# Kernel optimization log

Measured on AMD Instinct MI355X. Metric: run time of the kernel, lower is better.

Reference implementation:

```python
import jax, jax.numpy as jnp
import numpy as np
import math

BS, N, D_MODEL, H = 8, 1024, 512, 8
D_K = D_MODEL // H


def setup_inputs() -> dict:
    key = jax.random.key(0)
    ks = jax.random.split(key, 12)
    s = 1.0 / math.sqrt(D_MODEL)
    inp = {
        "query": jax.random.normal(ks[0], (BS, N, D_MODEL), jnp.float32),
        "key": jax.random.normal(ks[1], (BS, N, D_MODEL), jnp.float32),
        "value": jax.random.normal(ks[2], (BS, N, D_MODEL), jnp.float32),
        "wc_matrix": jax.random.normal(ks[3], (BS, N, N), jnp.float32),
        "Wq": jax.random.normal(ks[4], (D_MODEL, D_MODEL), jnp.float32) * s,
        "bq": jnp.zeros((D_MODEL,), jnp.float32),
        "Wk": jax.random.normal(ks[5], (D_MODEL, D_MODEL), jnp.float32) * s,
        "bk": jnp.zeros((D_MODEL,), jnp.float32),
        "Wv": jax.random.normal(ks[6], (D_MODEL, D_MODEL), jnp.float32) * s,
        "bv": jnp.zeros((D_MODEL,), jnp.float32),
        "Wo": jax.random.normal(ks[7], (D_MODEL, D_MODEL), jnp.float32) * s,
        "bo": jnp.zeros((D_MODEL,), jnp.float32),
    }
    return inp


def _split_heads(x):
    # (bs, N, d_model) -> (bs, h, N, d_k)
    b, n, _ = x.shape
    return x.reshape(b, n, H, D_K).transpose(0, 2, 1, 3)


def reference(query, key, value, wc_matrix, Wq, bq, Wk, bk, Wv, bv, Wo, bo):
    # Linear projections (torch Linear: x @ W.T + b), split into heads
    q = _split_heads(query @ Wq.T + bq)
    k = _split_heads(key @ Wk.T + bk)
    v = _split_heads(value @ Wv.T + bv)

    # scores: (bs, h, N, N)
    scores = jnp.einsum("bhnd,bhmd->bhnm", q, k) / jnp.sqrt(jnp.float32(D_K))
    # WC modulation: scores * softmax(wc)[:, None] + scores  (softmax_wc=True, residual=True)
    wc_sm = jax.nn.softmax(wc_matrix, axis=-1)[:, None]  # (bs, 1, N, N)
    scores = scores * wc_sm + scores
    p_attn = jax.nn.softmax(scores, axis=-1)  # dropout is identity in eval

    a = jnp.einsum("bhnm,bhmd->bhnd", p_attn, v)
    a = a.transpose(0, 2, 1, 3).reshape(query.shape[0], -1, D_MODEL)
    return a @ Wo.T + bo
```

## Files before the change

### kernel.cpp

```cpp
#include <hip/hip_runtime.h>
#include <math.h>


#define BS 8
#define SEQ 1024
#define DM 512
#define NH 8
#define DK 64
#define ROWS (BS * SEQ)

typedef __bf16 bf16_t;
typedef bf16_t bf16x8 __attribute__((ext_vector_type(8)));
typedef bf16_t bf16x4 __attribute__((ext_vector_type(4)));
typedef float f32x4 __attribute__((ext_vector_type(4)));

__device__ inline f32x4 mfma32(bf16x8 a, bf16x8 b, f32x4 c) {
  return __builtin_amdgcn_mfma_f32_16x16x32_bf16(a, b, c, 0, 0, 0);
}

__device__ inline void gload_lds16(const bf16_t* g, bf16_t* l) {
  __builtin_amdgcn_global_load_lds(
      (const __attribute__((address_space(1))) void*)g,
      (__attribute__((address_space(3))) void*)l, 16, 0, 0);
}

__global__ __launch_bounds__(256) void prep_kernel(
    const float* q, const float* k, const float* v,
    const float* wq, const float* wk, const float* wv, const float* wo,
    bf16_t* xq, bf16_t* xk, bf16_t* xv,
    bf16_t* wqb, bf16_t* wkb, bf16_t* wvb, bf16_t* wob,
    const float* __restrict__ wc, bf16_t* __restrict__ G) {
  int bx = blockIdx.x;
  int t = threadIdx.x;
  if (bx < 1664) {
    const float* srcs[7] = {q, k, v, wq, wk, wv, wo};
    bf16_t* dsts[7] = {xq, xk, xv, wqb, wkb, wvb, wob};
    int seg, boff;
    if (bx < 1536) { seg = bx >> 9; boff = bx & 511; }
    else { seg = 3 + ((bx - 1536) >> 5); boff = (bx - 1536) & 31; }
    const float* src = srcs[seg] + (size_t)boff * 8192;
    bf16_t* dst = dsts[seg] + (size_t)boff * 8192;
#pragma unroll
    for (int f = 0; f < 8; ++f) {
      int idx = (f * 256 + t) * 4;
      float4 x = *(const float4*)(src + idx);
      bf16x4 o;
      o[0] = (bf16_t)x.x; o[1] = (bf16_t)x.y; o[2] = (bf16_t)x.z; o[3] = (bf16_t)x.w;
      *(bf16x4*)(dst + idx) = o;
    }
  } else {
    int row = bx - 1664;
    const float* x = wc + (size_t)row * SEQ;
    bf16_t* y = G + (size_t)row * SEQ;
    float4 vv = *(const float4*)(x + t * 4);
    float m = fmaxf(fmaxf(vv.x, vv.y), fmaxf(vv.z, vv.w));
#pragma unroll
    for (int off = 32; off > 0; off >>= 1) m = fmaxf(m, __shfl_xor(m, off, 64));
    __shared__ float sm[4], ss[4];
    int w = t >> 6;
    if ((t & 63) == 0) sm[w] = m;
    __syncthreads();
    m = fmaxf(fmaxf(sm[0], sm[1]), fmaxf(sm[2], sm[3]));
    float4 e;
    e.x = __expf(vv.x - m); e.y = __expf(vv.y - m);
    e.z = __expf(vv.z - m); e.w = __expf(vv.w - m);
    float s = e.x + e.y + e.z + e.w;
#pragma unroll
    for (int off = 32; off > 0; off >>= 1) s += __shfl_xor(s, off, 64);
    if ((t & 63) == 0) ss[w] = s;
    __syncthreads();
    s = ss[0] + ss[1] + ss[2] + ss[3];
    float inv = 1.0f / s;
    const float SC = 0.18033688011112042f;
    bf16x4 g;
    g[0] = (bf16_t)((1.0f + e.x * inv) * SC);
    g[1] = (bf16_t)((1.0f + e.y * inv) * SC);
    g[2] = (bf16_t)((1.0f + e.z * inv) * SC);
    g[3] = (bf16_t)((1.0f + e.w * inv) * SC);
    *(bf16x4*)(y + t * 4) = g;
  }
}

template <int BM, bool WO>
__device__ inline void gemm_core(const bf16_t* X, const bf16_t* W,
                                 const float* bias, void* Cv,
                                 int mblk, int nblk, bool vtrans) {
  constexpr int STAGE_B = (2 * BM * 32 + 2 * 128 * 32) * 2;
  constexpr int EPI_B = WO ? BM * 132 * 4 : 128 * 136 * 2;
  constexpr int SMEM_B = STAGE_B > EPI_B ? STAGE_B : EPI_B;
  __shared__ __align__(16) char smem[SMEM_B];
  bf16_t* As = (bf16_t*)smem;
  bf16_t* Bs = (bf16_t*)smem + 2 * BM * 32;

  int t = threadIdx.x, lane = t & 63, w = t >> 6;
  int quad = lane >> 4, l15 = lane & 15;
  constexpr int MT = BM / 32;
  int m0w = (w & 1) * (BM / 2), n0w = (w >> 1) * 64;
  int mbase = mblk * BM, nbase = nblk * 128;
  int lr = lane >> 2, l4 = lane & 3;
  f32x4 acc[MT][4] = {};

#pragma unroll
  for (int f = 0; f < BM / 64; ++f) {
    int i = f * 4 + w;
    gload_lds16(X + (size_t)(mbase + i * 16 + lr) * DM + l4 * 8, &As[i * 512]);
  }
#pragma unroll
  for (int f = 0; f < 2; ++f) {
    int i = f * 4 + w;
    gload_lds16(W + (size_t)(nbase + i * 16 + lr) * DM + l4 * 8, &Bs[i * 512]);
  }

  for (int it = 0; it < 16; ++it) {
    __syncthreads();
    int cb = it & 1;
    if (it + 1 < 16) {
      int kb = (it + 1) * 32, nb = (it + 1) & 1;
#pragma unroll
      for (int f = 0; f < BM / 64; ++f) {
        int i = f * 4 + w;
        gload_lds16(X + (size_t)(mbase + i * 16 + lr) * DM + kb + l4 * 8,
                    &As[nb * BM * 32 + i * 512]);
      }
#pragma unroll
      for (int f = 0; f < 2; ++f) {
        int i = f * 4 + w;
        gload_lds16(W + (size_t)(nbase + i * 16 + lr) * DM + kb + l4 * 8,
                    &Bs[nb * 128 * 32 + i * 512]);
      }
    }
    bf16x8 af[MT], bfr[4];
#pragma unroll
    for (int mt = 0; mt < MT; ++mt)
      af[mt] = *(const bf16x8*)&As[cb * BM * 32 + (m0w + mt * 16 + l15) * 32 + quad * 8];
#pragma unroll
    for (int nt = 0; nt < 4; ++nt)
      bfr[nt] = *(const bf16x8*)&Bs[cb * 128 * 32 + (n0w + nt * 16 + l15) * 32 + quad * 8];
#pragma unroll
    for (int mt = 0; mt < MT; ++mt)
#pragma unroll
      for (int nt = 0; nt < 4; ++nt)
        acc[mt][nt] = mfma32(af[mt], bfr[nt], acc[mt][nt]);
  }

  if (WO) {
    __syncthreads();
    float* Cs = (float*)smem;
#pragma unroll
    for (int nt = 0; nt < 4; ++nt) {
      int colL = n0w + nt * 16 + l15;
      float bc = bias[nbase + colL];
#pragma unroll
      for (int mt = 0; mt < MT; ++mt)
#pragma unroll
        for (int r = 0; r < 4; ++r)
          Cs[(m0w + mt * 16 + quad * 4 + r) * 132 + colL] = acc[mt][nt][r] + bc;
    }
    __syncthreads();
    constexpr int NP = BM * 128 / 4 / 256;
#pragma unroll
    for (int p = 0; p < NP; ++p) {
      int flat = p * 256 + t;
      int row = flat >> 5, c4 = (flat & 31) * 4;
      float4 vv = *(const float4*)&Cs[row * 132 + c4];
      *(float4*)&((float*)Cv)[(size_t)(mbase + row) * DM + nbase + c4] = vv;
    }
  } else if (vtrans) {
    __syncthreads();
    bf16_t* Ts = (bf16_t*)smem;
#pragma unroll
    for (int nt = 0; nt < 4; ++nt) {
      int colL = n0w + nt * 16 + l15;
      float bc = bias[nbase + colL];
#pragma unroll
      for (int mt = 0; mt < MT; ++mt) {
        bf16x4 ov;
#pragma unroll
        for (int r = 0; r < 4; ++r) ov[r] = (bf16_t)(acc[mt][nt][r] + bc);
        *(bf16x4*)&Ts[colL * 136 + m0w + mt * 16 + quad * 4] = ov;
      }
    }
    __syncthreads();
    int b = mbase >> 10;
    int m0 = mbase & 1023;
#pragma unroll
    for (int p = 0; p < 8; ++p) {
      int flat = p * 256 + t;
      int colL = flat >> 4, m8 = (flat & 15) * 8;
      bf16x8 vv = *(const bf16x8*)&Ts[colL * 136 + m8];
      int colG = nbase + colL;
      int hh = colG >> 6, dd = colG & 63;
      *(bf16x8*)&((bf16_t*)Cv)[((size_t)(b * NH + hh) * DK + dd) * SEQ + m0 + m8] = vv;
    }
  } else {
#pragma unroll
    for (int nt = 0; nt < 4; ++nt) {
      int col = nbase + n0w + nt * 16 + l15;
      float bc = bias[col];
#pragma unroll
      for (int mt = 0; mt < MT; ++mt)
#pragma unroll
        for (int r = 0; r < 4; ++r) {
          int row = mbase + m0w + mt * 16 + quad * 4 + r;
          ((bf16_t*)Cv)[(size_t)row * DM + col] = (bf16_t)(acc[mt][nt][r] + bc);
        }
    }
  }
}

__global__ __launch_bounds__(256) void gemm_qkv_kernel(
    const bf16_t* xq, const bf16_t* xk, const bf16_t* xv,
    const bf16_t* wq, const bf16_t* wk, const bf16_t* wv,
    const float* bq, const float* bk, const float* bv,
    bf16_t* cq, bf16_t* ck, bf16_t* vt) {
  const bf16_t* Xarr[3] = {xq, xk, xv};
  const bf16_t* Warr[3] = {wq, wk, wv};
  const float* barr[3] = {bq, bk, bv};
  bf16_t* Carr[3] = {cq, ck, vt};
  int z = blockIdx.z;
  gemm_core<128, false>(Xarr[z], Warr[z], barr[z], Carr[z],
                        blockIdx.x, blockIdx.y, z == 2);
}

__global__ __launch_bounds__(256) void gemm_wo_kernel(const bf16_t* X, const bf16_t* W,
                                                      const float* bias, float* C) {
  gemm_core<64, true>(X, W, bias, C, blockIdx.x, blockIdx.y, false);
}

__global__ __launch_bounds__(256, 4) void flash_mfma_kernel(
    const bf16_t* __restrict__ Qb, const bf16_t* __restrict__ Kb,
    const bf16_t* __restrict__ Vt, const bf16_t* __restrict__ G,
    bf16_t* __restrict__ Ab) {
  int flat = blockIdx.x + 16 * (blockIdx.y + 8 * blockIdx.z);
  int l = (flat & 7) * 128 + (flat >> 3);
  int qt = l & 15, h = (l >> 4) & 7, b = l >> 7;

  __shared__ bf16_t Ks[2][64 * 64];
  __shared__ bf16_t Vs[2][64 * 64];
  __shared__ bf16_t Ps[4][16 * 64];
  int t = threadIdx.x, lane = t & 63, w = t >> 6;
  int quad = lane >> 4, l15 = lane & 15;
  int k7 = l15 & 7;

  int srow[2], scol[2];
#pragma unroll
  for (int f = 0; f < 2; ++f) {
    int idx = f * 256 + t;
    int r = idx >> 3, p = idx & 7;
    srow[f] = r;
    scol[f] = ((p ^ (r & 7)) * 8);
  }
  const bf16_t* Kbase = Kb + (size_t)(b * SEQ) * DM + h * DK;
  const bf16_t* Vbase = Vt + (size_t)((b * NH + h) * DK) * SEQ;

  size_t qrow_g = (size_t)(b * SEQ + qt * 64 + w * 16 + l15) * DM + h * DK;
  bf16x8 aq0 = *(const bf16x8*)&Qb[qrow_g + quad * 8];
  bf16x8 aq1 = *(const bf16x8*)&Qb[qrow_g + 32 + quad * 8];

  const size_t grow = (size_t)(b * SEQ + qt * 64 + w * 16 + l15) * SEQ;
  bf16x4 greg[4];
#pragma unroll
  for (int ct = 0; ct < 4; ++ct)
    greg[ct] = *(const bf16x4*)&G[grow + ct * 16 + quad * 4];

#pragma unroll
  for (int f = 0; f < 2; ++f) {
    int cbase = (f * 256 + w * 64) * 8;
    gload_lds16(Kbase + (size_t)srow[f] * DM + scol[f], &Ks[0][cbase]);
    gload_lds16(Vbase + (size_t)srow[f] * SEQ + scol[f], &Vs[0][cbase]);
  }
  asm volatile("s_waitcnt vmcnt(0)" ::: "memory");
  asm volatile("s_barrier" ::: "memory");

  float l_st = 0.f;
  f32x4 o[4] = {};

  for (int mt = 0; mt < 16; ++mt) {
    int cb = mt & 1;
    if (mt < 15) {
      int nb = cb ^ 1;
      const bf16_t* Kn = Kbase + (size_t)(mt + 1) * 64 * DM;
      const bf16_t* Vn = Vbase + (mt + 1) * 64;
#pragma unroll
      for (int f = 0; f < 2; ++f) {
        int cbase = (f * 256 + w * 64) * 8;
        gload_lds16(Kn + (size_t)srow[f] * DM + scol[f], &Ks[nb][cbase]);
        gload_lds16(Vn + (size_t)srow[f] * SEQ + scol[f], &Vs[nb][cbase]);
      }
      asm volatile("" ::: "memory");
    }

    f32x4 s[4];
    __builtin_amdgcn_s_setprio(1);
#pragma unroll
    for (int ct = 0; ct < 4; ++ct) {
      int r = ct * 16 + l15;
      int sw = r & 7;
      bf16x8 ak0 = *(const bf16x8*)&Ks[cb][r * 64 + ((quad ^ sw) * 8)];
      bf16x8 ak1 = *(const bf16x8*)&Ks[cb][r * 64 + (((4 + quad) ^ sw) * 8)];
      f32x4 z = {};
      s[ct] = mfma32(ak1, aq1, mfma32(ak0, aq0, z));
    }
    __builtin_amdgcn_s_setprio(0);

    float rs = 0.f;
#pragma unroll
    for (int ct = 0; ct < 4; ++ct) {
      bf16x4 pb;
#pragma unroll
      for (int r = 0; r < 4; ++r) {
        float p = __builtin_amdgcn_exp2f(s[ct][r] * (float)greg[ct][r]);
        pb[r] = (bf16_t)p;
        rs += p;
      }
      int chunk = (2 * ct + (quad >> 1)) ^ k7;
      *(bf16x4*)&Ps[w][l15 * 64 + chunk * 8 + (quad & 1) * 4] = pb;
    }
    if (mt < 15) {
#pragma unroll
      for (int ct = 0; ct < 4; ++ct)
        greg[ct] = *(const bf16x4*)&G[grow + (mt + 1) * 64 + ct * 16 + quad * 4];
    }
    rs += __shfl_xor(rs, 16, 64);
    rs += __shfl_xor(rs, 32, 64);
    l_st += rs;

    __builtin_amdgcn_s_setprio(1);
#pragma unroll
    for (int c = 0; c < 2; ++c) {
      int pchunk = (4 * c + quad) ^ k7;
      bf16x8 bp = *(const bf16x8*)&Ps[w][l15 * 64 + pchunk * 8];
#pragma unroll
      for (int dt = 0; dt < 4; ++dt) {
        int d = dt * 16 + l15;
        int vchunk = (4 * c + quad) ^ (d & 7);
        bf16x8 av = *(const bf16x8*)&Vs[cb][d * 64 + vchunk * 8];
        o[dt] = mfma32(av, bp, o[dt]);
      }
    }
    __builtin_amdgcn_s_setprio(0);

    if (mt < 15) {
      asm volatile("s_waitcnt vmcnt(4)" ::: "memory");
      asm volatile("s_barrier" ::: "memory");
    }
  }

  float linv = 1.0f / l_st;
#pragma unroll
  for (int dt = 0; dt < 4; ++dt) {
    bf16x4 ov;
#pragma unroll
    for (int r = 0; r < 4; ++r) ov[r] = (bf16_t)(o[dt][r] * linv);
    *(bf16x4*)&Ab[qrow_g + dt * 16 + quad * 4] = ov;
  }
}

extern "C" void kernel_launch(void* const* d_in, const int* in_sizes, int n_in,
                              void* d_out, int out_size, void* d_ws, size_t ws_size,
                              hipStream_t stream) {
  const float* query = (const float*)d_in[0];
  const float* key = (const float*)d_in[1];
  const float* value = (const float*)d_in[2];
  const float* wc = (const float*)d_in[3];
  const float* Wq = (const float*)d_in[4];
  const float* bq = (const float*)d_in[5];
  const float* Wk = (const float*)d_in[6];
  const float* bk = (const float*)d_in[7];
  const float* Wv = (const float*)d_in[8];
  const float* bv = (const float*)d_in[9];
  const float* Wo = (const float*)d_in[10];
  const float* bo = (const float*)d_in[11];
  float* out = (float*)d_out;

  const size_t ACT = (size_t)ROWS * DM;
  const size_t WSZ = (size_t)DM * DM;
  bf16_t* Qb = (bf16_t*)d_ws;
  bf16_t* Kb = Qb + ACT;
  bf16_t* Vb = Kb + ACT;
  bf16_t* Vt = Vb + ACT;
  bf16_t* Ab = Vt + ACT;
  bf16_t* G = Ab + ACT;
  bf16_t* Xq = G + (size_t)BS * SEQ * SEQ;
  bf16_t* Xk = Xq + ACT;
  bf16_t* Xv = Xk + ACT;
  bf16_t* Wqb = Xv + ACT;
  bf16_t* Wkb = Wqb + WSZ;
  bf16_t* Wvb = Wkb + WSZ;
  bf16_t* Wob = Wvb + WSZ;

  prep_kernel<<<1664 + BS * SEQ, 256, 0, stream>>>(
      query, key, value, Wq, Wk, Wv, Wo,
      Xq, Xk, Xv, Wqb, Wkb, Wvb, Wob, wc, G);

  gemm_qkv_kernel<<<dim3(ROWS / 128, DM / 128, 3), 256, 0, stream>>>(
      Xq, Xk, Xv, Wqb, Wkb, Wvb, bq, bk, bv, Qb, Kb, Vt);

  flash_mfma_kernel<<<dim3(SEQ / 64, NH, BS), 256, 0, stream>>>(Qb, Kb, Vt, G, Ab);

  gemm_wo_kernel<<<dim3(ROWS / 64, DM / 128), 256, 0, stream>>>(Ab, Wob, bo, out);
}
```

Before: 210.9 us.

## Fuse fp32-to-bf16 activation conversion into QKV GEMM A-tile loading

The QKV projection GEMM now reads fp32 query/key/value directly, converting to bf16 in registers and writing to LDS with a register-prefetched double buffer. The separate prep pass over the three activation tensors, along with their bf16 staging buffers, is removed. This cuts one full write plus reread of the activations in bf16. In exchange, A-tile loads go through VGPRs instead of direct global-to-LDS loads, which raises register pressure and adds conversion work inside the GEMM loop.

```diff
diff --git a/kernel.cpp b/kernel.cpp
--- a/kernel.cpp
+++ b/kernel.cpp
@@ -25,19 +25,15 @@
 }
 
 __global__ __launch_bounds__(256) void prep_kernel(
-    const float* q, const float* k, const float* v,
     const float* wq, const float* wk, const float* wv, const float* wo,
-    bf16_t* xq, bf16_t* xk, bf16_t* xv,
     bf16_t* wqb, bf16_t* wkb, bf16_t* wvb, bf16_t* wob,
     const float* __restrict__ wc, bf16_t* __restrict__ G) {
   int bx = blockIdx.x;
   int t = threadIdx.x;
-  if (bx < 1664) {
-    const float* srcs[7] = {q, k, v, wq, wk, wv, wo};
-    bf16_t* dsts[7] = {xq, xk, xv, wqb, wkb, wvb, wob};
-    int seg, boff;
-    if (bx < 1536) { seg = bx >> 9; boff = bx & 511; }
-    else { seg = 3 + ((bx - 1536) >> 5); boff = (bx - 1536) & 31; }
+  if (bx < 128) {
+    const float* srcs[4] = {wq, wk, wv, wo};
+    bf16_t* dsts[4] = {wqb, wkb, wvb, wob};
+    int seg = bx >> 5, boff = bx & 31;
     const float* src = srcs[seg] + (size_t)boff * 8192;
     bf16_t* dst = dsts[seg] + (size_t)boff * 8192;
 #pragma unroll
@@ -49,7 +45,7 @@
       *(bf16x4*)(dst + idx) = o;
     }
   } else {
-    int row = bx - 1664;
+    int row = bx - 128;
     const float* x = wc + (size_t)row * SEQ;
     bf16_t* y = G + (size_t)row * SEQ;
     float4 vv = *(const float4*)(x + t * 4);
@@ -81,16 +77,158 @@
   }
 }
 
-template <int BM, bool WO>
-__device__ inline void gemm_core(const bf16_t* X, const bf16_t* W,
-                                 const float* bias, void* Cv,
-                                 int mblk, int nblk, bool vtrans) {
+__device__ inline void gemm_qkv_core(const float* X, const bf16_t* W,
+                                     const float* bias, bf16_t* Cv,
+                                     int mblk, int nblk, bool vtrans) {
+  constexpr int STAGE_B = (2 * 128 * 32 + 2 * 128 * 32) * 2;
+  constexpr int EPI_B = 128 * 136 * 2;
+  constexpr int SMEM_B = STAGE_B > EPI_B ? STAGE_B : EPI_B;
+  __shared__ __align__(16) char smem[SMEM_B];
+  bf16_t* As = (bf16_t*)smem;
+  bf16_t* Bs = (bf16_t*)smem + 2 * 128 * 32;
+
+  int t = threadIdx.x, lane = t & 63, w = t >> 6;
+  int quad = lane >> 4, l15 = lane & 15;
+  int m0w = (w & 1) * 64, n0w = (w >> 1) * 64;
+  int mbase = mblk * 128, nbase = nblk * 128;
+  int lr = lane >> 2, l4 = lane & 3;
+  f32x4 acc[4][4] = {};
+
+  int arow = t >> 1, ahalf = (t & 1) * 16;
+  const float* Xbase = X + (size_t)(mbase + arow) * DM + ahalf;
+
+  float4 arA[4], arB[4];
+  auto issueA = [&](int it, float4(&s)[4]) {
+    const float* p = Xbase + it * 32;
+#pragma unroll
+    for (int i = 0; i < 4; ++i) s[i] = *(const float4*)(p + i * 4);
+  };
+  auto writeA = [&](int buf, float4(&s)[4]) {
+    bf16x8 v0, v1;
+    v0[0] = (bf16_t)s[0].x; v0[1] = (bf16_t)s[0].y;
+    v0[2] = (bf16_t)s[0].z; v0[3] = (bf16_t)s[0].w;
+    v0[4] = (bf16_t)s[1].x; v0[5] = (bf16_t)s[1].y;
+    v0[6] = (bf16_t)s[1].z; v0[7] = (bf16_t)s[1].w;
+    v1[0] = (bf16_t)s[2].x; v1[1] = (bf16_t)s[2].y;
+    v1[2] = (bf16_t)s[2].z; v1[3] = (bf16_t)s[2].w;
+    v1[4] = (bf16_t)s[3].x; v1[5] = (bf16_t)s[3].y;
+    v1[6] = (bf16_t)s[3].z; v1[7] = (bf16_t)s[3].w;
+    bf16_t* dst = &As[buf * 4096 + arow * 32 + ahalf];
+    *(bf16x8*)dst = v0;
+    *(bf16x8*)(dst + 8) = v1;
+  };
+  auto stageB = [&](int it, int buf) {
+#pragma unroll
+    for (int f = 0; f < 2; ++f) {
+      int i = f * 4 + w;
+      gload_lds16(W + (size_t)(nbase + i * 16 + lr) * DM + it * 32 + l4 * 8,
+                  &Bs[buf * 4096 + i * 512]);
+    }
+  };
+  auto compute = [&](int cb) {
+    bf16x8 af[4], bfr[4];
+#pragma unroll
+    for (int mt = 0; mt < 4; ++mt)
+      af[mt] = *(const bf16x8*)&As[cb * 4096 + (m0w + mt * 16 + l15) * 32 + quad * 8];
+#pragma unroll
+    for (int nt = 0; nt < 4; ++nt)
+      bfr[nt] = *(const bf16x8*)&Bs[cb * 4096 + (n0w + nt * 16 + l15) * 32 + quad * 8];
+#pragma unroll
+    for (int mt = 0; mt < 4; ++mt)
+#pragma unroll
+      for (int nt = 0; nt < 4; ++nt)
+        acc[mt][nt] = mfma32(af[mt], bfr[nt], acc[mt][nt]);
+  };
+
+  issueA(0, arA);
+  stageB(0, 0);
+  issueA(1, arB);
+  writeA(0, arA);
+
+#pragma unroll 1
+  for (int it2 = 0; it2 < 16; it2 += 2) {
+    __syncthreads();
+    if (it2 + 1 < 16) {
+      stageB(it2 + 1, 1);
+      writeA(1, arB);
+      if (it2 + 2 < 16) issueA(it2 + 2, arA);
+    }
+    compute(0);
+    __syncthreads();
+    if (it2 + 2 < 16) {
+      stageB(it2 + 2, 0);
+      writeA(0, arA);
+      if (it2 + 3 < 16) issueA(it2 + 3, arB);
+    }
+    compute(1);
+  }
+
+  if (vtrans) {
+    __syncthreads();
+    bf16_t* Ts = (bf16_t*)smem;
+#pragma unroll
+    for (int nt = 0; nt < 4; ++nt) {
+      int colL = n0w + nt * 16 + l15;
+      float bc = bias[nbase + colL];
+#pragma unroll
+      for (int mt = 0; mt < 4; ++mt) {
+        bf16x4 ov;
+#pragma unroll
+        for (int r = 0; r < 4; ++r) ov[r] = (bf16_t)(acc[mt][nt][r] + bc);
+        *(bf16x4*)&Ts[colL * 136 + m0w + mt * 16 + quad * 4] = ov;
+      }
+    }
+    __syncthreads();
+    int b = mbase >> 10;
+    int m0 = mbase & 1023;
+#pragma unroll
+    for (int p = 0; p < 8; ++p) {
+      int flat = p * 256 + t;
+      int colL = flat >> 4, m8 = (flat & 15) * 8;
+      bf16x8 vv = *(const bf16x8*)&Ts[colL * 136 + m8];
+      int colG = nbase + colL;
+      int hh = colG >> 6, dd = colG & 63;
+      *(bf16x8*)&Cv[((size_t)(b * NH + hh) * DK + dd) * SEQ + m0 + m8] = vv;
+    }
+  } else {
+#pragma unroll
+    for (int nt = 0; nt < 4; ++nt) {
+      int col = nbase + n0w + nt * 16 + l15;
+      float bc = bias[col];
+#pragma unroll
+      for (int mt = 0; mt < 4; ++mt)
+#pragma unroll
+        for (int r = 0; r < 4; ++r) {
+          int row = mbase + m0w + mt * 16 + quad * 4 + r;
+          Cv[(size_t)row * DM + col] = (bf16_t)(acc[mt][nt][r] + bc);
+        }
+    }
+  }
+}
+
+__global__ __launch_bounds__(256) void gemm_qkv_kernel(
+    const float* q, const float* k, const float* v,
+    const bf16_t* wq, const bf16_t* wk, const bf16_t* wv,
+    const float* bq, const float* bk, const float* bv,
+    bf16_t* cq, bf16_t* ck, bf16_t* vt) {
+  const float* Xarr[3] = {q, k, v};
+  const bf16_t* Warr[3] = {wq, wk, wv};
+  const float* barr[3] = {bq, bk, bv};
+  bf16_t* Carr[3] = {cq, ck, vt};
+  int z = blockIdx.z;
+  gemm_qkv_core(Xarr[z], Warr[z], barr[z], Carr[z], blockIdx.x, blockIdx.y, z == 2);
+}
+
+__global__ __launch_bounds__(256) void gemm_wo_kernel(const bf16_t* X, const bf16_t* W,
+                                                      const float* bias, float* C) {
+  constexpr int BM = 64;
   constexpr int STAGE_B = (2 * BM * 32 + 2 * 128 * 32) * 2;
-  constexpr int EPI_B = WO ? BM * 132 * 4 : 128 * 136 * 2;
+  constexpr int EPI_B = BM * 132 * 4;
   constexpr int SMEM_B = STAGE_B > EPI_B ? STAGE_B : EPI_B;
   __shared__ __align__(16) char smem[SMEM_B];
   bf16_t* As = (bf16_t*)smem;
   bf16_t* Bs = (bf16_t*)smem + 2 * BM * 32;
+  int mblk = blockIdx.x, nblk = blockIdx.y;
 
   int t = threadIdx.x, lane = t & 63, w = t >> 6;
   int quad = lane >> 4, l15 = lane & 15;
@@ -143,88 +281,27 @@
         acc[mt][nt] = mfma32(af[mt], bfr[nt], acc[mt][nt]);
   }
 
-  if (WO) {
-    __syncthreads();
-    float* Cs = (float*)smem;
-#pragma unroll
-    for (int nt = 0; nt < 4; ++nt) {
-      int colL = n0w + nt * 16 + l15;
-      float bc = bias[nbase + colL];
-#pragma unroll
-      for (int mt = 0; mt < MT; ++mt)
-#pragma unroll
-        for (int r = 0; r < 4; ++r)
-          Cs[(m0w + mt * 16 + quad * 4 + r) * 132 + colL] = acc[mt][nt][r] + bc;
-    }
-    __syncthreads();
-    constexpr int NP = BM * 128 / 4 / 256;
-#pragma unroll
-    for (int p = 0; p < NP; ++p) {
-      int flat = p * 256 + t;
-      int row = flat >> 5, c4 = (flat & 31) * 4;
-      float4 vv = *(const float4*)&Cs[row * 132 + c4];
-      *(float4*)&((float*)Cv)[(size_t)(mbase + row) * DM + nbase + c4] = vv;
-    }
-  } else if (vtrans) {
-    __syncthreads();
-    bf16_t* Ts = (bf16_t*)smem;
-#pragma unroll
-    for (int nt = 0; nt < 4; ++nt) {
-      int colL = n0w + nt * 16 + l15;
-      float bc = bias[nbase + colL];
-#pragma unroll
-      for (int mt = 0; mt < MT; ++mt) {
-        bf16x4 ov;
-#pragma unroll
-        for (int r = 0; r < 4; ++r) ov[r] = (bf16_t)(acc[mt][nt][r] + bc);
-        *(bf16x4*)&Ts[colL * 136 + m0w + mt * 16 + quad * 4] = ov;
-      }
-    }
-    __syncthreads();
-    int b = mbase >> 10;
-    int m0 = mbase & 1023;
-#pragma unroll
-    for (int p = 0; p < 8; ++p) {
-      int flat = p * 256 + t;
-      int colL = flat >> 4, m8 = (flat & 15) * 8;
-      bf16x8 vv = *(const bf16x8*)&Ts[colL * 136 + m8];
-      int colG = nbase + colL;
-      int hh = colG >> 6, dd = colG & 63;
-      *(bf16x8*)&((bf16_t*)Cv)[((size_t)(b * NH + hh) * DK + dd) * SEQ + m0 + m8] = vv;
-    }
-  } else {
-#pragma unroll
-    for (int nt = 0; nt < 4; ++nt) {
-      int col = nbase + n0w + nt * 16 + l15;
-      float bc = bias[col];
-#pragma unroll
-      for (int mt = 0; mt < MT; ++mt)
-#pragma unroll
-        for (int r = 0; r < 4; ++r) {
-          int row = mbase + m0w + mt * 16 + quad * 4 + r;
-          ((bf16_t*)Cv)[(size_t)row * DM + col] = (bf16_t)(acc[mt][nt][r] + bc);
-        }
-    }
-  }
-}
-
-__global__ __launch_bounds__(256) void gemm_qkv_kernel(
-    const bf16_t* xq, const bf16_t* xk, const bf16_t* xv,
-    const bf16_t* wq, const bf16_t* wk, const bf16_t* wv,
-    const float* bq, const float* bk, const float* bv,
-    bf16_t* cq, bf16_t* ck, bf16_t* vt) {
-  const bf16_t* Xarr[3] = {xq, xk, xv};
-  const bf16_t* Warr[3] = {wq, wk, wv};
-  const float* barr[3] = {bq, bk, bv};
-  bf16_t* Carr[3] = {cq, ck, vt};
-  int z = blockIdx.z;
-  gemm_core<128, false>(Xarr[z], Warr[z], barr[z], Carr[z],
-                        blockIdx.x, blockIdx.y, z == 2);
-}
-
-__global__ __launch_bounds__(256) void gemm_wo_kernel(const bf16_t* X, const bf16_t* W,
-                                                      const float* bias, float* C) {
-  gemm_core<64, true>(X, W, bias, C, blockIdx.x, blockIdx.y, false);
+  __syncthreads();
+  float* Cs = (float*)smem;
+#pragma unroll
+  for (int nt = 0; nt < 4; ++nt) {
+    int colL = n0w + nt * 16 + l15;
+    float bc = bias[nbase + colL];
+#pragma unroll
+    for (int mt = 0; mt < MT; ++mt)
+#pragma unroll
+      for (int r = 0; r < 4; ++r)
+        Cs[(m0w + mt * 16 + quad * 4 + r) * 132 + colL] = acc[mt][nt][r] + bc;
+  }
+  __syncthreads();
+  constexpr int NP = BM * 128 / 4 / 256;
+#pragma unroll
+  for (int p = 0; p < NP; ++p) {
+    int flat = p * 256 + t;
+    int row = flat >> 5, c4 = (flat & 31) * 4;
+    float4 vv = *(const float4*)&Cs[row * 132 + c4];
+    *(float4*)&C[(size_t)(mbase + row) * DM + nbase + c4] = vv;
+  }
 }
 
 __global__ __launch_bounds__(256, 4) void flash_mfma_kernel(
@@ -381,20 +458,16 @@
   bf16_t* Vt = Vb + ACT;
   bf16_t* Ab = Vt + ACT;
   bf16_t* G = Ab + ACT;
-  bf16_t* Xq = G + (size_t)BS * SEQ * SEQ;
-  bf16_t* Xk = Xq + ACT;
-  bf16_t* Xv = Xk + ACT;
-  bf16_t* Wqb = Xv + ACT;
+  bf16_t* Wqb = G + (size_t)BS * SEQ * SEQ;
   bf16_t* Wkb = Wqb + WSZ;
   bf16_t* Wvb = Wkb + WSZ;
   bf16_t* Wob = Wvb + WSZ;
 
-  prep_kernel<<<1664 + BS * SEQ, 256, 0, stream>>>(
-      query, key, value, Wq, Wk, Wv, Wo,
-      Xq, Xk, Xv, Wqb, Wkb, Wvb, Wob, wc, G);
+  prep_kernel<<<128 + BS * SEQ, 256, 0, stream>>>(
+      Wq, Wk, Wv, Wo, Wqb, Wkb, Wvb, Wob, wc, G);
 
   gemm_qkv_kernel<<<dim3(ROWS / 128, DM / 128, 3), 256, 0, stream>>>(
-      Xq, Xk, Xv, Wqb, Wkb, Wvb, bq, bk, bv, Qb, Kb, Vt);
+      query, key, value, Wqb, Wkb, Wvb, bq, bk, bv, Qb, Kb, Vt);
 
   flash_mfma_kernel<<<dim3(SEQ / 64, NH, BS), 256, 0, stream>>>(Qb, Kb, Vt, G, Ab);
 
```

Measured after the change: 231.5 us. 9.8% more time.
